# Optimization experiments

Hardware: AMD Instinct MI355X
Metric: run time of the kernel (lower is better)

The kernel has to match this reference:

```python
import jax, jax.numpy as jnp
import numpy as np
from jax import lax

HIDDEN = 128  # input_dim == hidden_dim


def skew(x):
    """Shift row i right by i. [B,C,H,W] -> [B,C,H,W+H-1]."""
    B, C, H, W = x.shape
    Ws = W + H - 1
    rows = jnp.arange(H)[:, None]
    cols = jnp.arange(Ws)[None, :]
    src = cols - rows                      # source col in unskewed map
    valid = (src >= 0) & (src < W)
    idx = jnp.clip(src, 0, W - 1)[None, None]
    g = jnp.take_along_axis(x, jnp.broadcast_to(idx, (B, C, H, Ws)), axis=3)
    return jnp.where(valid[None, None], g, jnp.zeros((), x.dtype))


def unskew(y, W):
    """Inverse of skew. [B,C,H,W+H-1] -> [B,C,H,W]."""
    B, C, H, Ws = y.shape
    idx = (jnp.arange(W)[None, :] + jnp.arange(H)[:, None])[None, None]
    return jnp.take_along_axis(y, jnp.broadcast_to(idx, (B, C, H, W)), axis=3)


def setup_inputs() -> dict:
    key = jax.random.key(0)
    k1, k2, k3 = jax.random.split(key, 3)
    C = HIDDEN
    x = jax.random.normal(k1, (16, C, 64, 64), dtype=jnp.float32)
    w_is = jax.random.normal(k2, (4 * C, C), dtype=jnp.float32) * (1.0 / np.sqrt(C))
    b_is = jnp.zeros((4 * C,), dtype=jnp.float32)
    w_ss = jax.random.normal(k3, (4 * C, C, 2), dtype=jnp.float32) * (1.0 / np.sqrt(2 * C))
    b_ss = jnp.zeros((4 * C,), dtype=jnp.float32)
    return {"x": x, "w_is": w_is, "b_is": b_is, "w_ss": w_ss, "b_ss": b_ss}


def reference(x, w_is, b_is, w_ss, b_ss):
    B, C, H, W = x.shape
    xs = skew(x)                                             # [B,C,H,Ws]
    # input-to-state: 1x1 (mask-B) conv -> 4C gate channels
    i_s = jnp.einsum('oi,bihw->bohw', w_is, xs) + b_is[None, :, None, None]

    def step(carry, ist):                                    # ist: [B,4C,H]
        h, c = carry                                         # [B,C,H]
        # state-to-state conv1d over height, kernel 2, one leading zero pad
        h_shift = jnp.pad(h, ((0, 0), (0, 0), (1, 0)))[:, :, :-1]
        s_s = (jnp.einsum('oi,bih->boh', w_ss[:, :, 0], h_shift)
               + jnp.einsum('oi,bih->boh', w_ss[:, :, 1], h)
               + b_ss[None, :, None])
        gates = ist + s_s                                    # [B,4C,H]
        ofi = jax.nn.sigmoid(gates[:, :3 * C])
        o, f, ig = ofi[:, :C], ofi[:, C:2 * C], ofi[:, 2 * C:]
        g = jnp.tanh(gates[:, 3 * C:])
        c_new = f * c + ig * g
        h_new = o * jnp.tanh(c_new)
        return (h_new, c_new), h_new

    h0 = jnp.zeros((B, C, H), dtype=x.dtype)
    c0 = jnp.zeros((B, C, H), dtype=x.dtype)
    i_s_t = jnp.moveaxis(i_s, 3, 0)                          # [Ws,B,4C,H]
    _, hs = lax.scan(step, (h0, c0), i_s_t)                  # hs: [Ws,B,C,H]
    out = jnp.moveaxis(hs, 0, 3)                             # [B,C,H,Ws]
    return unskew(out, W)
```

## Files before the change

### kernel.cpp

```cpp
#include <hip/hip_runtime.h>
#include <math.h>

namespace {

constexpr int B = 16, C = 128, H = 64, W = 64;
constexpr int T = W + H - 1;
constexpr int VSL = 33;

typedef short bf16x8 __attribute__((ext_vector_type(8)));
typedef float f32x4  __attribute__((ext_vector_type(4)));

__device__ __forceinline__ float4 ld_h16(const float* p) {
    unsigned long long a = __hip_atomic_load((const unsigned long long*)p,
                                             __ATOMIC_RELAXED, __HIP_MEMORY_SCOPE_AGENT);
    unsigned long long b = __hip_atomic_load(((const unsigned long long*)p) + 1,
                                             __ATOMIC_RELAXED, __HIP_MEMORY_SCOPE_AGENT);
    float4 r;
    r.x = __uint_as_float((unsigned)(a & 0xffffffffu));
    r.y = __uint_as_float((unsigned)(a >> 32));
    r.z = __uint_as_float((unsigned)(b & 0xffffffffu));
    r.w = __uint_as_float((unsigned)(b >> 32));
    return r;
}

__device__ __forceinline__ void stw(short* hi_p, short* lo_p, int base, float4 f) {
    unsigned ua = __float_as_uint(f.x), ub = __float_as_uint(f.y);
    unsigned h0 = (ua >> 16) | (ub & 0xffff0000u);
    float ra = f.x - __uint_as_float(ua & 0xffff0000u);
    float rb = f.y - __uint_as_float(ub & 0xffff0000u);
    unsigned l0 = (__float_as_uint(ra) >> 16) | (__float_as_uint(rb) & 0xffff0000u);
    unsigned uc = __float_as_uint(f.z), ud = __float_as_uint(f.w);
    unsigned h1 = (uc >> 16) | (ud & 0xffff0000u);
    float rc = f.z - __uint_as_float(uc & 0xffff0000u);
    float rd = f.w - __uint_as_float(ud & 0xffff0000u);
    unsigned l1 = (__float_as_uint(rc) >> 16) | (__float_as_uint(rd) & 0xffff0000u);
    *(uint2*)&hi_p[base] = make_uint2(h0, h1);
    *(uint2*)&lo_p[base] = make_uint2(l0, l1);
}

__global__ void transpose_x(const float* __restrict__ x, float* __restrict__ xT) {
    __shared__ float tile[C][W + 1];
    int b = blockIdx.x >> 6, row = blockIdx.x & 63;
    int tid = threadIdx.x;
#pragma unroll
    for (int i = 0; i < (C * W) / 256; ++i) {
        int idx = i * 256 + tid;
        int c = idx >> 6, w = idx & 63;
        tile[c][w] = x[((b * C + c) * H + row) * W + w];
    }
    __syncthreads();
#pragma unroll
    for (int i = 0; i < (C * W) / 256; ++i) {
        int idx = i * 256 + tid;
        int w = idx >> 7, c = idx & 127;
        xT[((b * H + row) * W + w) * C + c] = tile[c][w];
    }
}

__global__ __launch_bounds__(512, 2) void lstm_mfma(
        const float* __restrict__ xT,
        const float* __restrict__ w_is, const float* __restrict__ b_is,
        const float* __restrict__ w_ss, const float* __restrict__ b_ss,
        float* __restrict__ hist, unsigned int* __restrict__ flags) {

    __shared__ short vhi[48 * VSL * 8];
    __shared__ short vlo[48 * VSL * 8];

    const int tid  = threadIdx.x;
    const int og   = blockIdx.x & 7;
    const int pg   = blockIdx.x >> 3;
    const int pgm1 = (pg + 31) & 31;
    const int wave = tid >> 6;
    const int l    = tid & 63;
    const int ct   = wave >> 1;
    const int colhalf = wave & 1;

    const int rtile = l & 15;
    const int chl   = rtile >> 2;
    const int gate  = rtile & 3;
    const int khi   = l >> 4;
    const int co_a  = og * 16 + ct * 4 + chl;
    const int wrow  = gate * 128 + co_a;

    bf16x8 Ah[12], Al[12];
#pragma unroll
    for (int cc = 0; cc < 12; ++cc) {
#pragma unroll
        for (int j = 0; j < 8; ++j) {
            const int k = cc * 32 + khi * 8 + j;
            float val;
            if (k < 128)      val = w_is[wrow * 128 + k];
            else if (k < 256) val = w_ss[(wrow * 128 + (k - 128)) * 2 + 0];
            else              val = w_ss[(wrow * 128 + (k - 256)) * 2 + 1];
            const unsigned uv = __float_as_uint(val);
            Ah[cc][j] = (short)(uv >> 16);
            const float r = val - __uint_as_float(uv & 0xffff0000u);
            Al[cc][j] = (short)(__float_as_uint(r) >> 16);
        }
    }

    const int slot = (l & 15) + colhalf * 16;
    const int bO   = slot >> 1;
    const int rowO = pg + 32 * (slot & 1);
    const int chO  = og * 16 + ct * 4 + khi;
    float creg = 0.f;
    f32x4 bias;
#pragma unroll
    for (int g = 0; g < 4; ++g) bias[g] = b_is[g * 128 + chO] + b_ss[g * 128 + chO];

    const int lm   = (l < 32) ? l : (l - 32);
    const int kq_s = (lm >> 1) & 3;
    const int j0_s = (lm & 1) * 4;
    const int ccx  = lm >> 3;
    const int cch  = 8 + (lm >> 3);
    const int ccs  = 4 + (lm >> 3);

#pragma unroll 1
    for (int t = 0; t < T; ++t) {
        const bool any = ((unsigned)(t - pg) < 64u) | ((unsigned)(t - pg - 32) < 64u);

        float4 xr[4];
        if (any) {
#pragma unroll
            for (int i = 0; i < 4; ++i) {
                const int s   = wave * 4 + i;
                const int row = pg + 32 * (s & 1);
                const int w   = t - row;
                xr[i] = make_float4(0.f, 0.f, 0.f, 0.f);
                if ((unsigned)w < 64u && l < 32) {
                    const int b = s >> 1;
                    xr[i] = *(const float4*)&xT[((size_t)((b * H + row) * W) + w) * C + l * 4];
                }
            }
        }

        if (any && t > 0) {
            if (tid < 16) {
                const int qg = (tid < 8) ? pg : pgm1;
                const unsigned fidx = (unsigned)(qg * 8 + (tid & 7)) * 32u;
                while (__hip_atomic_load(&flags[fidx], __ATOMIC_RELAXED,
                                         __HIP_MEMORY_SCOPE_AGENT) < (unsigned)t) {}
            }
        }
        __syncthreads();

        if (any) {
#pragma unroll
            for (int i = 0; i < 4; ++i) {
                const int s   = wave * 4 + i;
                const int row = pg + 32 * (s & 1);
                const int w   = t - row;
                if ((unsigned)w < 64u) {
                    const int b = s >> 1;
                    const size_t posbase = ((size_t)((b * H + row) * W) + w) * C;
                    if (l < 32) {
                        stw(vhi, vlo, ((ccx * 4 + kq_s) * VSL + s) * 8 + j0_s, xr[i]);
                        float4 hv = make_float4(0.f, 0.f, 0.f, 0.f);
                        if (w > 0) hv = ld_h16(&hist[posbase - C + l * 4]);
                        stw(vhi, vlo, ((cch * 4 + kq_s) * VSL + s) * 8 + j0_s, hv);
                    } else {
                        float4 hs = make_float4(0.f, 0.f, 0.f, 0.f);
                        if (row > 0)
                            hs = ld_h16(&hist[((size_t)((b * H + row - 1) * W) + w) * C + lm * 4]);
                        stw(vhi, vlo, ((ccs * 4 + kq_s) * VSL + s) * 8 + j0_s, hs);
                    }
                }
            }
        }
        __syncthreads();

        if (any) {
            f32x4 acc = bias;
#pragma unroll
            for (int cc = 0; cc < 12; ++cc) {
                const int base = ((cc * 4 + khi) * VSL + slot) * 8;
                const bf16x8 Bh = *(const bf16x8*)&vhi[base];
                const bf16x8 Bl = *(const bf16x8*)&vlo[base];
                acc = __builtin_amdgcn_mfma_f32_16x16x32_bf16(Ah[cc], Bh, acc, 0, 0, 0);
                acc = __builtin_amdgcn_mfma_f32_16x16x32_bf16(Al[cc], Bh, acc, 0, 0, 0);
                acc = __builtin_amdgcn_mfma_f32_16x16x32_bf16(Ah[cc], Bl, acc, 0, 0, 0);
            }
            if ((unsigned)(t - rowO) < 64u) {
                const int w = t - rowO;
                const size_t posbase = ((size_t)((bO * H + rowO) * W) + w) * C;
                const float o_ = 1.f / (1.f + __expf(-acc[0]));
                const float f_ = 1.f / (1.f + __expf(-acc[1]));
                const float i_ = 1.f / (1.f + __expf(-acc[2]));
                const float g_ = tanhf(acc[3]);
                creg = f_ * creg + i_ * g_;
                const float hn = o_ * tanhf(creg);
                __hip_atomic_store(&hist[posbase + chO], hn,
                                   __ATOMIC_RELAXED, __HIP_MEMORY_SCOPE_AGENT);
            }
        }
        __syncthreads();
        if (tid == 0)
            __hip_atomic_store(&flags[(unsigned)(pg * 8 + og) * 32u], (unsigned)(t + 1),
                               __ATOMIC_RELAXED, __HIP_MEMORY_SCOPE_AGENT);
    }
}

__global__ void unhist(const float* __restrict__ hist, float* __restrict__ out) {
    __shared__ float tile[W][C + 1];
    int b = blockIdx.x >> 6, row = blockIdx.x & 63;
    int tid = threadIdx.x;
#pragma unroll
    for (int i = 0; i < (C * W) / 256; ++i) {
        int idx = i * 256 + tid;
        int w = idx >> 7, c = idx & 127;
        tile[w][c] = hist[((size_t)(b * H + row) * W + w) * C + c];
    }
    __syncthreads();
#pragma unroll
    for (int i = 0; i < (C * W) / 256; ++i) {
        int idx = i * 256 + tid;
        int c = idx >> 6, w = idx & 63;
        out[((size_t)(b * C + c) * H + row) * W + w] = tile[w][c];
    }
}

}

extern "C" void kernel_launch(void* const* d_in, const int* in_sizes, int n_in,
                              void* d_out, int out_size, void* d_ws, size_t ws_size,
                              hipStream_t stream) {
    const float* x    = (const float*)d_in[0];
    const float* w_is = (const float*)d_in[1];
    const float* b_is = (const float*)d_in[2];
    const float* w_ss = (const float*)d_in[3];
    const float* b_ss = (const float*)d_in[4];
    float* out = (float*)d_out;

    float* wsf  = (float*)d_ws;
    float* xT   = wsf;
    float* hist = xT + (size_t)B * H * W * C;
    unsigned int* flags = (unsigned int*)(hist + (size_t)B * H * W * C);

    hipLaunchKernelGGL(transpose_x, dim3(B * H), dim3(256), 0, stream, x, xT);
    hipMemsetAsync(flags, 0, 256 * 32 * sizeof(unsigned int), stream);

    void* args[] = { (void*)&xT, (void*)&w_is, (void*)&b_is, (void*)&w_ss,
                     (void*)&b_ss, (void*)&hist, (void*)&flags };
    hipLaunchCooperativeKernel((const void*)lstm_mfma, dim3(256), dim3(512),
                               args, 0, stream);

    hipLaunchKernelGGL(unhist, dim3(B * H), dim3(256), 0, stream, hist, out);
}
```

Baseline: 694.2 us.

## Hoist input-to-state GEMM out of recurrent loop into parallel pre-pass

Replaces the x transpose kernel with a fully parallel pre_gemm kernel that computes the input-to-state gate projections (plus biases) for all positions using split-bf16 MFMA. The recurrent cooperative kernel now only multiplies the state-to-state weights (K=256 instead of 384) and loads the precomputed gate values as its accumulator's starting value. This shortens the serial per-step critical path and frees register space. In exchange it adds a 4C-wide intermediate buffer (about 4x the size of x) that has to be written and then read back.

```diff
diff --git a/kernel.cpp b/kernel.cpp
--- a/kernel.cpp
+++ b/kernel.cpp
@@ -5,7 +5,8 @@
 
 constexpr int B = 16, C = 128, H = 64, W = 64;
 constexpr int T = W + H - 1;
-constexpr int VSL = 33;
+constexpr int SL  = 264;
+constexpr int XSL = 136;
 
 typedef short bf16x8 __attribute__((ext_vector_type(8)));
 typedef float f32x4  __attribute__((ext_vector_type(4)));
@@ -21,6 +22,13 @@
     r.z = __uint_as_float((unsigned)(b & 0xffffffffu));
     r.w = __uint_as_float((unsigned)(b >> 32));
     return r;
+}
+
+__device__ __forceinline__ void split1(float v, short& hh, short& ll) {
+    const unsigned u = __float_as_uint(v);
+    hh = (short)(u >> 16);
+    const float r = v - __uint_as_float(u & 0xffff0000u);
+    ll = (short)(__float_as_uint(r) >> 16);
 }
 
 __device__ __forceinline__ void stw(short* hi_p, short* lo_p, int base, float4 f) {
@@ -38,33 +46,78 @@
     *(uint2*)&lo_p[base] = make_uint2(l0, l1);
 }
 
-__global__ void transpose_x(const float* __restrict__ x, float* __restrict__ xT) {
-    __shared__ float tile[C][W + 1];
-    int b = blockIdx.x >> 6, row = blockIdx.x & 63;
-    int tid = threadIdx.x;
-#pragma unroll
-    for (int i = 0; i < (C * W) / 256; ++i) {
-        int idx = i * 256 + tid;
-        int c = idx >> 6, w = idx & 63;
-        tile[c][w] = x[((b * C + c) * H + row) * W + w];
+__global__ __launch_bounds__(512) void pre_gemm(
+        const float* __restrict__ x, const float* __restrict__ w_is,
+        const float* __restrict__ b_is, const float* __restrict__ b_ss,
+        float* __restrict__ is_out) {
+    __shared__ short xhi[32 * XSL];
+    __shared__ short xlo[32 * XSL];
+    __shared__ float ot[32][68];
+
+    const int og   = blockIdx.x & 7;
+    const int pgrp = blockIdx.x >> 3;
+    const int b    = pgrp >> 7;
+    const int row  = (pgrp >> 1) & 63;
+    const int w0   = (pgrp & 1) * 32;
+    const int tid  = threadIdx.x;
+    const int wave = tid >> 6, l = tid & 63;
+    const int ct = wave >> 1, colhalf = wave & 1;
+    const int rtile = l & 15, khi = l >> 4;
+    const int chl = rtile >> 2, gate = rtile & 3;
+    const int wrow = gate * 128 + og * 16 + ct * 4 + chl;
+
+    bf16x8 Ah[4], Al[4];
+#pragma unroll
+    for (int cc = 0; cc < 4; ++cc)
+#pragma unroll
+        for (int j = 0; j < 8; ++j) {
+            short hh, ll;
+            split1(w_is[wrow * 128 + cc * 32 + khi * 8 + j], hh, ll);
+            Ah[cc][j] = hh; Al[cc][j] = ll;
+        }
+
+#pragma unroll
+    for (int it = 0; it < 2; ++it) {
+        const int idx = it * 512 + tid;
+        const int c = idx >> 3, wq = (idx & 7) * 4;
+        const float4 xv = *(const float4*)&x[((size_t)(b * C + c) * H + row) * W + w0 + wq];
+        short hh, ll;
+        split1(xv.x, hh, ll); xhi[(wq + 0) * XSL + c] = hh; xlo[(wq + 0) * XSL + c] = ll;
+        split1(xv.y, hh, ll); xhi[(wq + 1) * XSL + c] = hh; xlo[(wq + 1) * XSL + c] = ll;
+        split1(xv.z, hh, ll); xhi[(wq + 2) * XSL + c] = hh; xlo[(wq + 2) * XSL + c] = ll;
+        split1(xv.w, hh, ll); xhi[(wq + 3) * XSL + c] = hh; xlo[(wq + 3) * XSL + c] = ll;
     }
     __syncthreads();
-#pragma unroll
-    for (int i = 0; i < (C * W) / 256; ++i) {
-        int idx = i * 256 + tid;
-        int w = idx >> 7, c = idx & 127;
-        xT[((b * H + row) * W + w) * C + c] = tile[c][w];
-    }
+
+    const int slot = (l & 15) + colhalf * 16;
+    const int cl   = ct * 4 + khi;
+    const int chO  = og * 16 + cl;
+    f32x4 acc;
+#pragma unroll
+    for (int g = 0; g < 4; ++g) acc[g] = b_is[g * 128 + chO] + b_ss[g * 128 + chO];
+#pragma unroll
+    for (int cc = 0; cc < 4; ++cc) {
+        const int base = slot * XSL + cc * 32 + khi * 8;
+        const bf16x8 Bh = *(const bf16x8*)&xhi[base];
+        const bf16x8 Bl = *(const bf16x8*)&xlo[base];
+        acc = __builtin_amdgcn_mfma_f32_16x16x32_bf16(Ah[cc], Bh, acc, 0, 0, 0);
+        acc = __builtin_amdgcn_mfma_f32_16x16x32_bf16(Al[cc], Bh, acc, 0, 0, 0);
+        acc = __builtin_amdgcn_mfma_f32_16x16x32_bf16(Ah[cc], Bl, acc, 0, 0, 0);
+    }
+    *(f32x4*)&ot[slot][cl * 4] = acc;
+    __syncthreads();
+
+    const int p2 = tid >> 4, j2 = tid & 15;
+    const size_t pos = (size_t)pgrp * 32 + p2;
+    *(float4*)&is_out[pos * 512 + og * 64 + j2 * 4] = *(const float4*)&ot[p2][j2 * 4];
 }
 
 __global__ __launch_bounds__(512, 2) void lstm_mfma(
-        const float* __restrict__ xT,
-        const float* __restrict__ w_is, const float* __restrict__ b_is,
-        const float* __restrict__ w_ss, const float* __restrict__ b_ss,
+        const float* __restrict__ is_in, const float* __restrict__ w_ss,
         float* __restrict__ hist, unsigned int* __restrict__ flags) {
 
-    __shared__ short vhi[48 * VSL * 8];
-    __shared__ short vlo[48 * VSL * 8];
+    __shared__ short vhi[32 * SL];
+    __shared__ short vlo[32 * SL];
 
     const int tid  = threadIdx.x;
     const int og   = blockIdx.x & 7;
@@ -75,63 +128,39 @@
     const int ct   = wave >> 1;
     const int colhalf = wave & 1;
 
-    const int rtile = l & 15;
-    const int chl   = rtile >> 2;
-    const int gate  = rtile & 3;
-    const int khi   = l >> 4;
-    const int co_a  = og * 16 + ct * 4 + chl;
-    const int wrow  = gate * 128 + co_a;
-
-    bf16x8 Ah[12], Al[12];
-#pragma unroll
-    for (int cc = 0; cc < 12; ++cc) {
+    const int rtile = l & 15, khi = l >> 4;
+    const int chl = rtile >> 2, gate = rtile & 3;
+    const int wrow = gate * 128 + og * 16 + ct * 4 + chl;
+
+    bf16x8 Ah[8], Al[8];
+#pragma unroll
+    for (int cc = 0; cc < 8; ++cc)
 #pragma unroll
         for (int j = 0; j < 8; ++j) {
             const int k = cc * 32 + khi * 8 + j;
-            float val;
-            if (k < 128)      val = w_is[wrow * 128 + k];
-            else if (k < 256) val = w_ss[(wrow * 128 + (k - 128)) * 2 + 0];
-            else              val = w_ss[(wrow * 128 + (k - 256)) * 2 + 1];
-            const unsigned uv = __float_as_uint(val);
-            Ah[cc][j] = (short)(uv >> 16);
-            const float r = val - __uint_as_float(uv & 0xffff0000u);
-            Al[cc][j] = (short)(__float_as_uint(r) >> 16);
-        }
-    }
+            const float val = (k < 128) ? w_ss[(wrow * 128 + k) * 2 + 0]
+                                        : w_ss[(wrow * 128 + (k - 128)) * 2 + 1];
+            short hh, ll; split1(val, hh, ll);
+            Ah[cc][j] = hh; Al[cc][j] = ll;
+        }
 
     const int slot = (l & 15) + colhalf * 16;
     const int bO   = slot >> 1;
     const int rowO = pg + 32 * (slot & 1);
-    const int chO  = og * 16 + ct * 4 + khi;
+    const int cl   = ct * 4 + khi;
+    const int chO  = og * 16 + cl;
+    const int lm   = l & 31;
     float creg = 0.f;
-    f32x4 bias;
-#pragma unroll
-    for (int g = 0; g < 4; ++g) bias[g] = b_is[g * 128 + chO] + b_ss[g * 128 + chO];
-
-    const int lm   = (l < 32) ? l : (l - 32);
-    const int kq_s = (lm >> 1) & 3;
-    const int j0_s = (lm & 1) * 4;
-    const int ccx  = lm >> 3;
-    const int cch  = 8 + (lm >> 3);
-    const int ccs  = 4 + (lm >> 3);
 
 #pragma unroll 1
     for (int t = 0; t < T; ++t) {
-        const bool any = ((unsigned)(t - pg) < 64u) | ((unsigned)(t - pg - 32) < 64u);
-
-        float4 xr[4];
-        if (any) {
-#pragma unroll
-            for (int i = 0; i < 4; ++i) {
-                const int s   = wave * 4 + i;
-                const int row = pg + 32 * (s & 1);
-                const int w   = t - row;
-                xr[i] = make_float4(0.f, 0.f, 0.f, 0.f);
-                if ((unsigned)w < 64u && l < 32) {
-                    const int b = s >> 1;
-                    xr[i] = *(const float4*)&xT[((size_t)((b * H + row) * W) + w) * C + l * 4];
-                }
-            }
+        const bool any  = ((unsigned)(t - pg) < 64u) | ((unsigned)(t - pg - 32) < 64u);
+        const bool actO = (unsigned)(t - rowO) < 64u;
+
+        f32x4 is4 = {0.f, 0.f, 0.f, 0.f};
+        if (actO) {
+            const size_t pos = (size_t)(bO * H + rowO) * W + (t - rowO);
+            is4 = *(const f32x4*)&is_in[pos * 512 + og * 64 + cl * 4];
         }
 
         if (any && t > 0) {
@@ -152,17 +181,16 @@
                 const int w   = t - row;
                 if ((unsigned)w < 64u) {
                     const int b = s >> 1;
-                    const size_t posbase = ((size_t)((b * H + row) * W) + w) * C;
                     if (l < 32) {
-                        stw(vhi, vlo, ((ccx * 4 + kq_s) * VSL + s) * 8 + j0_s, xr[i]);
                         float4 hv = make_float4(0.f, 0.f, 0.f, 0.f);
-                        if (w > 0) hv = ld_h16(&hist[posbase - C + l * 4]);
-                        stw(vhi, vlo, ((cch * 4 + kq_s) * VSL + s) * 8 + j0_s, hv);
+                        if (row > 0)
+                            hv = ld_h16(&hist[((size_t)(b * H + row - 1) * W + w) * C + lm * 4]);
+                        stw(vhi, vlo, s * SL + lm * 4, hv);
                     } else {
-                        float4 hs = make_float4(0.f, 0.f, 0.f, 0.f);
-                        if (row > 0)
-                            hs = ld_h16(&hist[((size_t)((b * H + row - 1) * W) + w) * C + lm * 4]);
-                        stw(vhi, vlo, ((ccs * 4 + kq_s) * VSL + s) * 8 + j0_s, hs);
+                        float4 hp = make_float4(0.f, 0.f, 0.f, 0.f);
+                        if (w > 0)
+                            hp = ld_h16(&hist[((size_t)(b * H + row) * W + (w - 1)) * C + lm * 4]);
+                        stw(vhi, vlo, s * SL + 128 + lm * 4, hp);
                     }
                 }
             }
@@ -170,19 +198,19 @@
         __syncthreads();
 
         if (any) {
-            f32x4 acc = bias;
-#pragma unroll
-            for (int cc = 0; cc < 12; ++cc) {
-                const int base = ((cc * 4 + khi) * VSL + slot) * 8;
+            f32x4 acc = is4;
+#pragma unroll
+            for (int cc = 0; cc < 8; ++cc) {
+                const int base = slot * SL + cc * 32 + khi * 8;
                 const bf16x8 Bh = *(const bf16x8*)&vhi[base];
                 const bf16x8 Bl = *(const bf16x8*)&vlo[base];
                 acc = __builtin_amdgcn_mfma_f32_16x16x32_bf16(Ah[cc], Bh, acc, 0, 0, 0);
                 acc = __builtin_amdgcn_mfma_f32_16x16x32_bf16(Al[cc], Bh, acc, 0, 0, 0);
                 acc = __builtin_amdgcn_mfma_f32_16x16x32_bf16(Ah[cc], Bl, acc, 0, 0, 0);
             }
-            if ((unsigned)(t - rowO) < 64u) {
+            if (actO) {
                 const int w = t - rowO;
-                const size_t posbase = ((size_t)((bO * H + rowO) * W) + w) * C;
+                const size_t posbase = ((size_t)(bO * H + rowO) * W + w) * C;
                 const float o_ = 1.f / (1.f + __expf(-acc[0]));
                 const float f_ = 1.f / (1.f + __expf(-acc[1]));
                 const float i_ = 1.f / (1.f + __expf(-acc[2]));
@@ -232,15 +260,15 @@
     float* out = (float*)d_out;
 
     float* wsf  = (float*)d_ws;
-    float* xT   = wsf;
-    float* hist = xT + (size_t)B * H * W * C;
+    float* is_b = wsf;
+    float* hist = is_b + (size_t)B * H * W * 512;
     unsigned int* flags = (unsigned int*)(hist + (size_t)B * H * W * C);
 
-    hipLaunchKernelGGL(transpose_x, dim3(B * H), dim3(256), 0, stream, x, xT);
     hipMemsetAsync(flags, 0, 256 * 32 * sizeof(unsigned int), stream);
-
-    void* args[] = { (void*)&xT, (void*)&w_is, (void*)&b_is, (void*)&w_ss,
-                     (void*)&b_ss, (void*)&hist, (void*)&flags };
+    hipLaunchKernelGGL(pre_gemm, dim3(2048 * 8), dim3(512), 0, stream,
+                       x, w_is, b_is, b_ss, is_b);
+
+    void* args[] = { (void*)&is_b, (void*)&w_ss, (void*)&hist, (void*)&flags };
     hipLaunchCooperativeKernel((const void*)lstm_mfma, dim3(256), dim3(512),
                                args, 0, stream);
 
```

Result: slower. 753.2 us (+8.5%).
